# Kernel optimization log

Measured on AMD Instinct MI355X. Metric: run time of the kernel, lower is better.

## Reference

```python
import jax, jax.numpy as jnp
import numpy as np

B, S, D, H = 2, 2048, 1024, 16
HD = D // H
LOCAL_WINDOW = 32
GLOBAL_TOKENS = 16
BLOCK_SIZE = 64
SPARSITY = 0.75


def _structured_mask(seq_len):
    """local_global | block_sparse pattern, vectorized numpy (deterministic)."""
    i = np.arange(seq_len)[:, None]
    j = np.arange(seq_len)[None, :]
    half = LOCAL_WINDOW // 2
    local = np.abs(i - j) <= half  # mask[i, i-16 : i+17]
    glob = (i < GLOBAL_TOKENS) | (j < GLOBAL_TOKENS)
    stride = max(1, seq_len // 64)
    strided = ((i % stride) == 0) & ((j % stride) == 0)
    lg = local | glob | strided
    # block sparse: random blocks kept with prob 1-SPARSITY, diagonal always kept
    nb = (seq_len + BLOCK_SIZE - 1) // BLOCK_SIZE
    rng = np.random.default_rng(0)
    block_mask = rng.random((nb, nb)) > SPARSITY
    np.fill_diagonal(block_mask, True)
    bs = np.kron(block_mask, np.ones((BLOCK_SIZE, BLOCK_SIZE), dtype=bool))[:seq_len, :seq_len]
    return lg | bs


def setup_inputs() -> dict:
    key = jax.random.key(0)
    ks = jax.random.split(key, 12)
    std = 1.0 / np.sqrt(D)
    inp = {
        'query': jax.random.normal(ks[0], (B, S, D), jnp.float32),
        'key': jax.random.normal(ks[1], (B, S, D), jnp.float32),
        'value': jax.random.normal(ks[2], (B, S, D), jnp.float32),
        'Wq': jax.random.normal(ks[3], (D, D), jnp.float32) * std,
        'bq': jnp.zeros((D,), jnp.float32),
        'Wk': jax.random.normal(ks[4], (D, D), jnp.float32) * std,
        'bk': jnp.zeros((D,), jnp.float32),
        'Wv': jax.random.normal(ks[5], (D, D), jnp.float32) * std,
        'bv': jnp.zeros((D,), jnp.float32),
        'Wo': jax.random.normal(ks[6], (D, D), jnp.float32) * std,
        'bo': jnp.zeros((D,), jnp.float32),
        'sparse_mask': jnp.asarray(_structured_mask(S)),
    }
    return inp


def reference(query, key, value, Wq, bq, Wk, bk, Wv, bv, Wo, bo, sparse_mask):
    scale = HD ** -0.5
    # projections -> [B, H, S, HD]
    q = (query @ Wq + bq).reshape(B, S, H, HD).transpose(0, 2, 1, 3)
    k = (key @ Wk + bk).reshape(B, S, H, HD).transpose(0, 2, 1, 3)
    v = (value @ Wv + bv).reshape(B, S, H, HD).transpose(0, 2, 1, 3)
    # dense scores then structured sparse mask (matches original math)
    scores = jnp.einsum('bhqd,bhkd->bhqk', q, k) * scale
    scores = jnp.where(sparse_mask[None, None], scores, -jnp.inf)
    attn = jax.nn.softmax(scores, axis=-1)  # every row has >=1 active entry (global cols)
    out = jnp.einsum('bhqk,bhkd->bhqd', attn, v)
    out = out.transpose(0, 2, 1, 3).reshape(B, S, D)
    out = out @ Wo + bo
    return out, attn
```

## Files before the change

kernel.cpp:

```cpp
#include <hip/hip_runtime.h>
#include <hip/hip_bf16.h>
#include <hip/hip_fp16.h>

using u16 = unsigned short;
using u32 = unsigned int;
using u64 = unsigned long long;

typedef __attribute__((ext_vector_type(8))) short short8;
typedef __attribute__((ext_vector_type(8))) _Float16 half8;
typedef __attribute__((ext_vector_type(4))) _Float16 half4;
typedef __attribute__((ext_vector_type(4))) float f32x4;
typedef __attribute__((ext_vector_type(2))) u32 u32x2;

#define DEVI static __device__ __forceinline__

DEVI float bfu2f(u16 u) { return __builtin_bit_cast(float, (u32)u << 16); }
DEVI u16 f2bfu(float f) { return __builtin_bit_cast(u16, __float2bfloat16(f)); }
DEVI u16 f2hu(float f) { return __builtin_bit_cast(u16, (_Float16)f); }

DEVI f32x4 mfma_f16_(half8 a, half8 b, f32x4 c) {
  return __builtin_amdgcn_mfma_f32_16x16x32_f16(a, b, c, 0, 0, 0);
}
DEVI f32x4 mfma16_f16_(half4 a, half4 b, f32x4 c) {
  return __builtin_amdgcn_mfma_f32_16x16x16f16(a, b, c, 0, 0, 0);
}

#define GLD_LDS16(src, dst) \
  __builtin_amdgcn_global_load_lds((const __attribute__((address_space(1))) void*)(src), \
                                   (__attribute__((address_space(3))) void*)(dst), 16, 0, 0)

#define BAR() __builtin_amdgcn_s_barrier()
#define VMCNT(n) asm volatile("s_waitcnt vmcnt(" #n ")" ::: "memory")

static constexpr int Bsz = 2, S = 2048, D = 1024, H = 16, HD = 64;
static constexpr int MROWS = Bsz * S;
static constexpr size_t OUT_ELEMS = (size_t)Bsz * S * D;
static constexpr float C_EXP2 = 0.18033688f;
static constexpr size_t OFF_WT  = 0;
static constexpr size_t OFF_Q   = 0x800000;
static constexpr size_t OFF_K   = 0x1000000;
static constexpr size_t OFF_V   = 0x1800000;
static constexpr size_t OFF_VT  = 0x2000000;
static constexpr size_t OFF_O   = 0x2800000;
static constexpr size_t OFF_MB  = 0x3000000;
static constexpr size_t OFF_FLG = 0x3080000;

__global__ __launch_bounds__(256) void detect_dtype(
    const u16* __restrict__ q, int* __restrict__ flag)
{
  __shared__ u32 red[256];
  const int tid = threadIdx.x;
  u32 mx = 0;
  for (int i = tid; i < 32768; i += 256) {
    u32 e = (q[2 * i] >> 7) & 0xFF;
    mx = mx > e ? mx : e;
  }
  red[tid] = mx;
  __syncthreads();
  if (tid == 0) {
    u32 m = 0;
    for (int i = 0; i < 256; ++i) m = m > red[i] ? m : red[i];
    flag[0] = (m >= 0x90) ? 1 : 0;
  }
}

__global__ __launch_bounds__(256) void conv_f16(
    const void* __restrict__ X, u16* __restrict__ Y, const int* __restrict__ flag)
{
  const size_t i8 = ((size_t)blockIdx.x * 256 + threadIdx.x) * 8;
  half8 o;
  if (*flag) {
    const float* x = (const float*)X + i8;
    float4 f0 = ((const float4*)x)[0], f1 = ((const float4*)x)[1];
    o[0] = (_Float16)f0.x; o[1] = (_Float16)f0.y;
    o[2] = (_Float16)f0.z; o[3] = (_Float16)f0.w;
    o[4] = (_Float16)f1.x; o[5] = (_Float16)f1.y;
    o[6] = (_Float16)f1.z; o[7] = (_Float16)f1.w;
  } else {
    uint4 a = *(const uint4*)((const u16*)X + i8);
    u32 wd[4] = {a.x, a.y, a.z, a.w};
    #pragma unroll
    for (int j = 0; j < 4; ++j) {
      o[2 * j]     = (_Float16)bfu2f((u16)(wd[j] & 0xFFFF));
      o[2 * j + 1] = (_Float16)bfu2f((u16)(wd[j] >> 16));
    }
  }
  *reinterpret_cast<half8*>(Y + i8) = o;
}

__global__ __launch_bounds__(256) void prep_w(
    const void* __restrict__ Wq, const void* __restrict__ Wk,
    const void* __restrict__ Wv, const void* __restrict__ Wo,
    u16* __restrict__ WT, const int* __restrict__ flag)
{
  __shared__ _Float16 t[64][80];
  const int z = blockIdx.z;
  const void* src = z == 0 ? Wq : z == 1 ? Wk : z == 2 ? Wv : Wo;
  u16* dst = WT + (size_t)z * 1024 * 1024;
  const int bx = blockIdx.x, by = blockIdx.y;
  const int tid = threadIdx.x;
  const int r = tid >> 2, ch = tid & 3;
  const int fl = *flag;
  if (fl) {
    const float* s = (const float*)src + (size_t)(by * 64 + r) * 1024 + bx * 64 + ch * 16;
    #pragma unroll
    for (int v = 0; v < 4; ++v) {
      float4 f = ((const float4*)s)[v];
      t[r][ch * 16 + v * 4 + 0] = (_Float16)f.x;
      t[r][ch * 16 + v * 4 + 1] = (_Float16)f.y;
      t[r][ch * 16 + v * 4 + 2] = (_Float16)f.z;
      t[r][ch * 16 + v * 4 + 3] = (_Float16)f.w;
    }
  } else {
    const u16* s = (const u16*)src + (size_t)(by * 64 + r) * 1024 + bx * 64 + ch * 16;
    uint4 a0 = ((const uint4*)s)[0], a1 = ((const uint4*)s)[1];
    u32 wds[8] = {a0.x, a0.y, a0.z, a0.w, a1.x, a1.y, a1.z, a1.w};
    #pragma unroll
    for (int j = 0; j < 8; ++j) {
      t[r][ch * 16 + 2 * j]     = (_Float16)bfu2f((u16)(wds[j] & 0xFFFF));
      t[r][ch * 16 + 2 * j + 1] = (_Float16)bfu2f((u16)(wds[j] >> 16));
    }
  }
  __syncthreads();
  half8 o0, o1;
  #pragma unroll
  for (int i = 0; i < 8; ++i) { o0[i] = t[ch * 16 + i][r]; o1[i] = t[ch * 16 + 8 + i][r]; }
  u16* d = dst + (size_t)(bx * 64 + r) * 1024 + by * 64 + ch * 16;
  *reinterpret_cast<half8*>(d) = o0;
  *reinterpret_cast<half8*>(d + 8) = o1;
}

__global__ __launch_bounds__(256) void mask_bits_kernel(
    const void* __restrict__ mask, u64* __restrict__ mbits)
{
  const u32 w0 = *(const u32*)mask;
  int mode;
  if (w0 == 0x01010101u) mode = 0;
  else if ((w0 & 0xFFFFu) && (w0 >> 16)) mode = 1;
  else mode = 2;
  const int row = blockIdx.x;
  const int w = threadIdx.x >> 6, l = threadIdx.x & 63;
  for (int i = 0; i < 8; ++i) {
    int jw = w * 8 + i;
    size_t idx = (size_t)row * S + jw * 64 + l;
    bool m;
    if (mode == 0)      m = ((const unsigned char*)mask)[idx] != 0;
    else if (mode == 1) m = ((const u16*)mask)[idx] != 0;
    else                m = ((const u32*)mask)[idx] != 0;
    u64 bal = __ballot(m);
    if (l == 0) mbits[(size_t)row * 32 + jw] = bal;
  }
}

template<int OUT_DYN>
__global__ __launch_bounds__(256) void gemm_f16(
    const _Float16* __restrict__ A, const _Float16* __restrict__ Bt,
    const void* __restrict__ bias, void* __restrict__ C,
    const int* __restrict__ flag, int M, int N, int K)
{
  __shared__ _Float16 As[64 * 64];
  __shared__ _Float16 Bs[128 * 64];
  const int tid = threadIdx.x;
  const int w = tid >> 6, l = tid & 63;
  const int wr = w >> 1, wc = w & 1;
  const int lg = l >> 4, lc = l & 15;
  const int tM = blockIdx.x * 64, tN = blockIdx.y * 128;
  const int fl = *flag;
  const int rr = l >> 3;
  const int gsw = (l & 7) ^ rr;
  const int rsw = lc & 7;

  f32x4 acc[2][4] = {};

  for (int k0 = 0; k0 < K; k0 += 64) {
    #pragma unroll
    for (int s = 0; s < 2; ++s)
      GLD_LDS16(A + (size_t)(tM + w * 16 + s * 8 + rr) * K + k0 + gsw * 8,
                &As[(w * 16 + s * 8) * 64]);
    #pragma unroll
    for (int s = 0; s < 4; ++s)
      GLD_LDS16(Bt + (size_t)(tN + w * 32 + s * 8 + rr) * K + k0 + gsw * 8,
                &Bs[(w * 32 + s * 8) * 64]);
    __syncthreads();
    half8 a[2][2], b[4][2];
    #pragma unroll
    for (int m = 0; m < 2; ++m)
      #pragma unroll
      for (int kk = 0; kk < 2; ++kk)
        a[m][kk] = *reinterpret_cast<const half8*>(
            &As[(wr * 32 + m * 16 + lc) * 64 + ((kk * 4 + lg) ^ rsw) * 8]);
    #pragma unroll
    for (int n = 0; n < 4; ++n)
      #pragma unroll
      for (int kk = 0; kk < 2; ++kk)
        b[n][kk] = *reinterpret_cast<const half8*>(
            &Bs[(wc * 64 + n * 16 + lc) * 64 + ((kk * 4 + lg) ^ rsw) * 8]);
    #pragma unroll
    for (int m = 0; m < 2; ++m)
      #pragma unroll
      for (int n = 0; n < 4; ++n) {
        acc[m][n] = mfma_f16_(a[m][0], b[n][0], acc[m][n]);
        acc[m][n] = mfma_f16_(a[m][1], b[n][1], acc[m][n]);
      }
    __syncthreads();
  }

  float bf[4];
  #pragma unroll
  for (int n = 0; n < 4; ++n) {
    int col = tN + wc * 64 + n * 16 + lc;
    bf[n] = fl ? ((const float*)bias)[col] : bfu2f(((const u16*)bias)[col]);
  }
  #pragma unroll
  for (int m = 0; m < 2; ++m) {
    int row = tM + wr * 32 + m * 16 + lg * 4;
    #pragma unroll
    for (int n = 0; n < 4; ++n) {
      int col = tN + wc * 64 + n * 16 + lc;
      #pragma unroll
      for (int r = 0; r < 4; ++r) {
        float v = acc[m][n][r] + bf[n];
        size_t off = (size_t)(row + r) * N + col;
        if (OUT_DYN) {
          if (fl) ((float*)C)[off] = v;
          else    ((u16*)C)[off] = f2bfu(v);
        } else {
          ((u16*)C)[off] = f2hu(v);
        }
      }
    }
  }
}

__global__ __launch_bounds__(256) void transpose_v(
    const _Float16* __restrict__ V, _Float16* __restrict__ vT)
{
  __shared__ _Float16 t[64][80];
  const int sb = blockIdx.x, bh = blockIdx.y;
  const int b = bh >> 4, h = bh & 15;
  const int tid = threadIdx.x;
  #pragma unroll
  for (int rep = 0; rep < 2; ++rep) {
    int idx = rep * 256 + tid;
    int sl = idx >> 3, ch = idx & 7;
    *reinterpret_cast<uint4*>(&t[sl][ch * 8]) =
      *reinterpret_cast<const uint4*>(V + (size_t)(b * S + sb * 64 + sl) * D + h * HD + ch * 8);
  }
  __syncthreads();
  #pragma unroll
  for (int rep = 0; rep < 2; ++rep) {
    int idx = rep * 256 + tid;
    int hd = idx >> 3, ch = idx & 7;
    half8 ov;
    #pragma unroll
    for (int i = 0; i < 8; ++i) ov[i] = t[ch * 8 + i][hd];
    *reinterpret_cast<half8*>(vT + ((size_t)bh * HD + hd) * S + sb * 64 + ch * 8) = ov;
  }
}

__global__ __launch_bounds__(256) void attn_kernel(
    const _Float16* __restrict__ Q, const _Float16* __restrict__ Kp,
    const _Float16* __restrict__ vT, const u64* __restrict__ mbits,
    _Float16* __restrict__ O, void* __restrict__ dOut,
    const int* __restrict__ flag)
{
  __shared__ _Float16 Ks[2][4096];
  __shared__ _Float16 Vs[2][4096];

  const int tid = threadIdx.x, w = tid >> 6, l = tid & 63;
  const int lg = l >> 4, lc = l & 15;
  const int flat = blockIdx.y * 32 + blockIdx.x;
  const int nf = (flat & 7) * 128 + (flat >> 3);
  const int rb = nf & 31, bh = nf >> 5;
  const int b = bh >> 4, h = bh & 15;
  const int wg = w ^ (rb & 1);
  const int wrow = rb * 64 + wg * 16;
  const int fl = *flag;

  half8 aq[2];
  {
    const _Float16* qp = Q + (size_t)(b * S + wrow + lc) * D + h * HD;
    aq[0] = *reinterpret_cast<const half8*>(qp + lg * 8);
    aq[1] = *reinterpret_cast<const half8*>(qp + 32 + lg * 8);
  }
  const _Float16* kbase = Kp + (size_t)(b * S) * D + h * HD;
  const _Float16* vbase = vT + (size_t)bh * HD * S;
  const u64* mrow = mbits + (size_t)(wrow + lc) * 32;

  const int rr = w * 8 + (l >> 3);
  const int gsw = (l & 7) ^ (rr & 7);

  #define STAGE_K(buf, jb) do { \
    const _Float16* s0_ = kbase + (size_t)((jb) * 64 + rr) * D + gsw * 8; \
    GLD_LDS16(s0_, &Ks[buf][w * 512]); \
    GLD_LDS16(s0_ + (size_t)32 * D, &Ks[buf][2048 + w * 512]); \
  } while (0)
  #define STAGE_V(buf, jb) do { \
    const _Float16* s0_ = vbase + (size_t)rr * S + (jb) * 64 + gsw * 8; \
    GLD_LDS16(s0_, &Vs[buf][w * 512]); \
    GLD_LDS16(s0_ + (size_t)32 * S, &Vs[buf][2048 + w * 512]); \
  } while (0)

  const int sw = lc & 7;

  float rs = 0.f;
  f32x4 accO[4] = {};

  STAGE_K(0, 0);
  STAGE_V(0, 0);
  u64 mb = mrow[0];

  #pragma unroll 1
  for (int jb = 0; jb < 32; ++jb) {
    const int buf = jb & 1;
    BAR();
    if (jb < 31) {
      STAGE_K(buf ^ 1, jb + 1);
      STAGE_V(buf ^ 1, jb + 1);
      VMCNT(5);
    } else {
      VMCNT(1);
    }
    BAR();
    const u64 mb_next = (jb < 31) ? mrow[jb + 1] : 0ull;
    const _Float16* kt = Ks[buf];
    const _Float16* vt = Vs[buf];
    #pragma unroll
    for (int c = 0; c < 4; ++c) {
      const u32 bits = (u32)(mb >> (c * 16 + lg * 4)) & 0xFu;
      if (__any(bits != 0)) {
        const int r = c * 16 + lc;
        half8 ka = *reinterpret_cast<const half8*>(&kt[r * 64 + ((lg ^ sw) * 8)]);
        half8 kb = *reinterpret_cast<const half8*>(&kt[r * 64 + (((lg + 4) ^ sw) * 8)]);
        f32x4 sc = {};
        sc = mfma_f16_(ka, aq[0], sc);
        sc = mfma_f16_(kb, aq[1], sc);
        half4 pa;
        #pragma unroll
        for (int r2 = 0; r2 < 4; ++r2) {
          float p = ((bits >> r2) & 1) ? exp2f(sc[r2] * C_EXP2) : 0.f;
          rs += p;
          pa[r2] = (_Float16)p;
        }
        #pragma unroll
        for (int d = 0; d < 4; ++d) {
          const int rd = d * 16 + lc;
          const int ch = (2 * c + (lg >> 1)) ^ sw;
          half4 vv = *reinterpret_cast<const half4*>(&vt[rd * 64 + ch * 8 + (lg & 1) * 4]);
          accO[d] = mfma16_f16_(pa, vv, accO[d]);
        }
      }
    }
    mb = mb_next;
  }

  rs += __shfl_xor(rs, 16);
  rs += __shfl_xor(rs, 32);
  const float inv = 1.f / rs;
  const float lg2i = -__log2f(rs);

  float invr[4];
  #pragma unroll
  for (int r = 0; r < 4; ++r) invr[r] = __shfl(inv, lg * 4 + r);

  {
    _Float16* op = O + (size_t)(b * S + wrow + lg * 4) * D + h * HD;
    #pragma unroll
    for (int d = 0; d < 4; ++d)
      #pragma unroll
      for (int r = 0; r < 4; ++r)
        op[(size_t)r * D + d * 16 + lc] = (_Float16)(accO[d][r] * invr[r]);
  }

  STAGE_K(0, 0);
  mb = mrow[0];

  if (fl) {
    float* ar = (float*)dOut + OUT_ELEMS + (size_t)bh * S * S + (size_t)(wrow + lc) * S;
    #pragma unroll 1
    for (int jb = 0; jb < 32; ++jb) {
      const int buf = jb & 1;
      BAR();
      if (jb < 31) { STAGE_K(buf ^ 1, jb + 1); VMCNT(7); }
      else VMCNT(5);
      BAR();
      const u64 mb_next = (jb < 31) ? mrow[jb + 1] : 0ull;
      const _Float16* kt = Ks[buf];
      #pragma unroll
      for (int c = 0; c < 4; ++c) {
        const u32 bits = (u32)(mb >> (c * 16 + lg * 4)) & 0xFu;
        f32x4* dst = (f32x4*)(ar + jb * 64 + c * 16 + lg * 4);
        if (__any(bits != 0)) {
          const int r = c * 16 + lc;
          half8 ka = *reinterpret_cast<const half8*>(&kt[r * 64 + ((lg ^ sw) * 8)]);
          half8 kb = *reinterpret_cast<const half8*>(&kt[r * 64 + (((lg + 4) ^ sw) * 8)]);
          f32x4 sc = {};
          sc = mfma_f16_(ka, aq[0], sc);
          sc = mfma_f16_(kb, aq[1], sc);
          f32x4 pv;
          #pragma unroll
          for (int r2 = 0; r2 < 4; ++r2)
            pv[r2] = ((bits >> r2) & 1) ? exp2f(__builtin_fmaf(sc[r2], C_EXP2, lg2i)) : 0.f;
          __builtin_nontemporal_store(pv, dst);
        } else {
          f32x4 z = {};
          __builtin_nontemporal_store(z, dst);
        }
      }
      mb = mb_next;
    }
  } else {
    u16* ar = (u16*)dOut + OUT_ELEMS + (size_t)bh * S * S + (size_t)(wrow + lc) * S;
    #pragma unroll 1
    for (int jb = 0; jb < 32; ++jb) {
      const int buf = jb & 1;
      BAR();
      if (jb < 31) { STAGE_K(buf ^ 1, jb + 1); VMCNT(7); }
      else VMCNT(5);
      BAR();
      const u64 mb_next = (jb < 31) ? mrow[jb + 1] : 0ull;
      const _Float16* kt = Ks[buf];
      #pragma unroll
      for (int c = 0; c < 4; ++c) {
        const u32 bits = (u32)(mb >> (c * 16 + lg * 4)) & 0xFu;
        u32x2* dst = (u32x2*)(ar + jb * 64 + c * 16 + lg * 4);
        if (__any(bits != 0)) {
          const int r = c * 16 + lc;
          half8 ka = *reinterpret_cast<const half8*>(&kt[r * 64 + ((lg ^ sw) * 8)]);
          half8 kb = *reinterpret_cast<const half8*>(&kt[r * 64 + (((lg + 4) ^ sw) * 8)]);
          f32x4 sc = {};
          sc = mfma_f16_(ka, aq[0], sc);
          sc = mfma_f16_(kb, aq[1], sc);
          float p0 = ((bits >> 0) & 1) ? exp2f(__builtin_fmaf(sc[0], C_EXP2, lg2i)) : 0.f;
          float p1 = ((bits >> 1) & 1) ? exp2f(__builtin_fmaf(sc[1], C_EXP2, lg2i)) : 0.f;
          float p2 = ((bits >> 2) & 1) ? exp2f(__builtin_fmaf(sc[2], C_EXP2, lg2i)) : 0.f;
          float p3 = ((bits >> 3) & 1) ? exp2f(__builtin_fmaf(sc[3], C_EXP2, lg2i)) : 0.f;
          u32x2 pk;
          pk[0] = (u32)f2bfu(p0) | ((u32)f2bfu(p1) << 16);
          pk[1] = (u32)f2bfu(p2) | ((u32)f2bfu(p3) << 16);
          __builtin_nontemporal_store(pk, dst);
        } else {
          u32x2 z = {0, 0};
          __builtin_nontemporal_store(z, dst);
        }
      }
      mb = mb_next;
    }
  }
  #undef STAGE_K
  #undef STAGE_V
}

extern "C" void kernel_launch(void* const* d_in, const int* in_sizes, int n_in,
                              void* d_out, int out_size, void* d_ws, size_t ws_size,
                              hipStream_t stream) {
  const void* query = d_in[0];
  const void* key_  = d_in[1];
  const void* value = d_in[2];
  const void* Wq = d_in[3];  const void* bq = d_in[4];
  const void* Wk = d_in[5];  const void* bk = d_in[6];
  const void* Wv = d_in[7];  const void* bv = d_in[8];
  const void* Wo = d_in[9];  const void* bo = d_in[10];
  const void* mask = d_in[11];

  char* ws = (char*)d_ws;
  u16* WT   = (u16*)(ws + OFF_WT);
  u16* Qb   = (u16*)(ws + OFF_Q);
  u16* Kb   = (u16*)(ws + OFF_K);
  u16* Vb   = (u16*)(ws + OFF_V);
  u16* vTb  = (u16*)(ws + OFF_VT);
  u16* Ob   = (u16*)(ws + OFF_O);
  u64* mbits = (u64*)(ws + OFF_MB);
  int* flag  = (int*)(ws + OFF_FLG);

  u16* WqT = WT, *WkT = WT + 1048576, *WvT = WT + 2097152, *WoT = WT + 3145728;
  u16* X = vTb;

  detect_dtype<<<1, 256, 0, stream>>>((const u16*)query, flag);
  prep_w<<<dim3(16, 16, 4), 256, 0, stream>>>(Wq, Wk, Wv, Wo, WT, flag);
  mask_bits_kernel<<<dim3(S), 256, 0, stream>>>(mask, mbits);

  const dim3 gg(MROWS / 64, D / 128);
  conv_f16<<<dim3(2048), 256, 0, stream>>>(query, X, flag);
  gemm_f16<0><<<gg, 256, 0, stream>>>((const _Float16*)X, (const _Float16*)WqT,
                                      bq, Qb, flag, MROWS, D, D);
  conv_f16<<<dim3(2048), 256, 0, stream>>>(key_, X, flag);
  gemm_f16<0><<<gg, 256, 0, stream>>>((const _Float16*)X, (const _Float16*)WkT,
                                      bk, Kb, flag, MROWS, D, D);
  conv_f16<<<dim3(2048), 256, 0, stream>>>(value, X, flag);
  gemm_f16<0><<<gg, 256, 0, stream>>>((const _Float16*)X, (const _Float16*)WvT,
                                      bv, Vb, flag, MROWS, D, D);

  transpose_v<<<dim3(32, 32), 256, 0, stream>>>((const _Float16*)Vb, (_Float16*)vTb);
  attn_kernel<<<dim3(32, 32), 256, 0, stream>>>(
      (const _Float16*)Qb, (const _Float16*)Kb, (const _Float16*)vTb,
      mbits, (_Float16*)Ob, d_out, flag);
  gemm_f16<1><<<gg, 256, 0, stream>>>((const _Float16*)Ob, (const _Float16*)WoT,
                                      bo, d_out, flag, MROWS, D, D);
}
```

Before: 344.9 us.

## Fuse input dtype conversion into a single batched QKV projection GEMM

The three separate conversion kernels and three projection GEMMs become one launch with a z-dimension of three. Each block converts fp32/bf16 activations to fp16 in registers and writes them straight into swizzled LDS, so the converted copy no longer makes a round trip through global memory. The A-tile load now goes through plain register loads instead of direct-to-LDS loads, which may lose some latency hiding. Separately, the attention-probability output stores switch from nontemporal to regular stores.

```diff
diff --git a/kernel.cpp b/kernel.cpp
--- a/kernel.cpp
+++ b/kernel.cpp
@@ -62,30 +62,6 @@
     for (int i = 0; i < 256; ++i) m = m > red[i] ? m : red[i];
     flag[0] = (m >= 0x90) ? 1 : 0;
   }
-}
-
-__global__ __launch_bounds__(256) void conv_f16(
-    const void* __restrict__ X, u16* __restrict__ Y, const int* __restrict__ flag)
-{
-  const size_t i8 = ((size_t)blockIdx.x * 256 + threadIdx.x) * 8;
-  half8 o;
-  if (*flag) {
-    const float* x = (const float*)X + i8;
-    float4 f0 = ((const float4*)x)[0], f1 = ((const float4*)x)[1];
-    o[0] = (_Float16)f0.x; o[1] = (_Float16)f0.y;
-    o[2] = (_Float16)f0.z; o[3] = (_Float16)f0.w;
-    o[4] = (_Float16)f1.x; o[5] = (_Float16)f1.y;
-    o[6] = (_Float16)f1.z; o[7] = (_Float16)f1.w;
-  } else {
-    uint4 a = *(const uint4*)((const u16*)X + i8);
-    u32 wd[4] = {a.x, a.y, a.z, a.w};
-    #pragma unroll
-    for (int j = 0; j < 4; ++j) {
-      o[2 * j]     = (_Float16)bfu2f((u16)(wd[j] & 0xFFFF));
-      o[2 * j + 1] = (_Float16)bfu2f((u16)(wd[j] >> 16));
-    }
-  }
-  *reinterpret_cast<half8*>(Y + i8) = o;
 }
 
 __global__ __launch_bounds__(256) void prep_w(
@@ -152,31 +128,59 @@
   }
 }
 
-template<int OUT_DYN>
-__global__ __launch_bounds__(256) void gemm_f16(
-    const _Float16* __restrict__ A, const _Float16* __restrict__ Bt,
-    const void* __restrict__ bias, void* __restrict__ C,
-    const int* __restrict__ flag, int M, int N, int K)
-{
-  __shared__ _Float16 As[64 * 64];
-  __shared__ _Float16 Bs[128 * 64];
+template<int A_DYN, int OUT_DYN>
+DEVI void gemm_body(const void* __restrict__ A, const _Float16* __restrict__ Bt,
+                    const void* __restrict__ bias, void* __restrict__ C,
+                    int fl, int tM, int tN, int N, int K,
+                    _Float16* As, _Float16* Bs)
+{
   const int tid = threadIdx.x;
   const int w = tid >> 6, l = tid & 63;
   const int wr = w >> 1, wc = w & 1;
   const int lg = l >> 4, lc = l & 15;
-  const int tM = blockIdx.x * 64, tN = blockIdx.y * 128;
-  const int fl = *flag;
   const int rr = l >> 3;
   const int gsw = (l & 7) ^ rr;
   const int rsw = lc & 7;
+  const int arow = tid >> 2, ach = tid & 3;
 
   f32x4 acc[2][4] = {};
 
   for (int k0 = 0; k0 < K; k0 += 64) {
-    #pragma unroll
-    for (int s = 0; s < 2; ++s)
-      GLD_LDS16(A + (size_t)(tM + w * 16 + s * 8 + rr) * K + k0 + gsw * 8,
-                &As[(w * 16 + s * 8) * 64]);
+    if (A_DYN) {
+      half8 h0, h1;
+      if (fl) {
+        const float* ap = (const float*)A + (size_t)(tM + arow) * K + k0 + ach * 16;
+        float4 f0 = ((const float4*)ap)[0], f1 = ((const float4*)ap)[1];
+        float4 f2 = ((const float4*)ap)[2], f3 = ((const float4*)ap)[3];
+        h0[0] = (_Float16)f0.x; h0[1] = (_Float16)f0.y;
+        h0[2] = (_Float16)f0.z; h0[3] = (_Float16)f0.w;
+        h0[4] = (_Float16)f1.x; h0[5] = (_Float16)f1.y;
+        h0[6] = (_Float16)f1.z; h0[7] = (_Float16)f1.w;
+        h1[0] = (_Float16)f2.x; h1[1] = (_Float16)f2.y;
+        h1[2] = (_Float16)f2.z; h1[3] = (_Float16)f2.w;
+        h1[4] = (_Float16)f3.x; h1[5] = (_Float16)f3.y;
+        h1[6] = (_Float16)f3.z; h1[7] = (_Float16)f3.w;
+      } else {
+        const u16* ap = (const u16*)A + (size_t)(tM + arow) * K + k0 + ach * 16;
+        uint4 a0 = ((const uint4*)ap)[0], a1 = ((const uint4*)ap)[1];
+        u32 wd[8] = {a0.x, a0.y, a0.z, a0.w, a1.x, a1.y, a1.z, a1.w};
+        #pragma unroll
+        for (int j = 0; j < 4; ++j) {
+          h0[2 * j]     = (_Float16)bfu2f((u16)(wd[j] & 0xFFFF));
+          h0[2 * j + 1] = (_Float16)bfu2f((u16)(wd[j] >> 16));
+          h1[2 * j]     = (_Float16)bfu2f((u16)(wd[4 + j] & 0xFFFF));
+          h1[2 * j + 1] = (_Float16)bfu2f((u16)(wd[4 + j] >> 16));
+        }
+      }
+      const int c0 = (2 * ach) ^ (arow & 7), c1 = (2 * ach + 1) ^ (arow & 7);
+      *reinterpret_cast<half8*>(&As[arow * 64 + c0 * 8]) = h0;
+      *reinterpret_cast<half8*>(&As[arow * 64 + c1 * 8]) = h1;
+    } else {
+      #pragma unroll
+      for (int s = 0; s < 2; ++s)
+        GLD_LDS16((const _Float16*)A + (size_t)(tM + w * 16 + s * 8 + rr) * K + k0 + gsw * 8,
+                  &As[(w * 16 + s * 8) * 64]);
+    }
     #pragma unroll
     for (int s = 0; s < 4; ++s)
       GLD_LDS16(Bt + (size_t)(tN + w * 32 + s * 8 + rr) * K + k0 + gsw * 8,
@@ -230,6 +234,36 @@
       }
     }
   }
+}
+
+__global__ __launch_bounds__(256) void gemm_qkv(
+    const void* __restrict__ Aq, const void* __restrict__ Ak,
+    const void* __restrict__ Av, const u16* __restrict__ WT,
+    const void* __restrict__ bq, const void* __restrict__ bk,
+    const void* __restrict__ bv,
+    u16* __restrict__ Qb, u16* __restrict__ Kb, u16* __restrict__ Vb,
+    const int* __restrict__ flag)
+{
+  __shared__ _Float16 As[64 * 64];
+  __shared__ _Float16 Bs[128 * 64];
+  const int z = blockIdx.z;
+  const void* A = z == 0 ? Aq : z == 1 ? Ak : Av;
+  const _Float16* Bt = (const _Float16*)(WT + (size_t)z * 1048576);
+  const void* bias = z == 0 ? bq : z == 1 ? bk : bv;
+  void* C = z == 0 ? Qb : z == 1 ? Kb : Vb;
+  gemm_body<1, 0>(A, Bt, bias, C, *flag,
+                  blockIdx.x * 64, blockIdx.y * 128, D, D, As, Bs);
+}
+
+__global__ __launch_bounds__(256) void gemm_o(
+    const _Float16* __restrict__ A, const u16* __restrict__ WoT,
+    const void* __restrict__ bias, void* __restrict__ C,
+    const int* __restrict__ flag)
+{
+  __shared__ _Float16 As[64 * 64];
+  __shared__ _Float16 Bs[128 * 64];
+  gemm_body<0, 1>(A, (const _Float16*)WoT, bias, C, *flag,
+                  blockIdx.x * 64, blockIdx.y * 128, D, D, As, Bs);
 }
 
 __global__ __launch_bounds__(256) void transpose_v(
@@ -401,10 +435,10 @@
           #pragma unroll
           for (int r2 = 0; r2 < 4; ++r2)
             pv[r2] = ((bits >> r2) & 1) ? exp2f(__builtin_fmaf(sc[r2], C_EXP2, lg2i)) : 0.f;
-          __builtin_nontemporal_store(pv, dst);
+          *dst = pv;
         } else {
           f32x4 z = {};
-          __builtin_nontemporal_store(z, dst);
+          *dst = z;
         }
       }
       mb = mb_next;
@@ -438,10 +472,10 @@
           u32x2 pk;
           pk[0] = (u32)f2bfu(p0) | ((u32)f2bfu(p1) << 16);
           pk[1] = (u32)f2bfu(p2) | ((u32)f2bfu(p3) << 16);
-          __builtin_nontemporal_store(pk, dst);
+          *dst = pk;
         } else {
           u32x2 z = {0, 0};
-          __builtin_nontemporal_store(z, dst);
+          *dst = z;
         }
       }
       mb = mb_next;
@@ -473,28 +507,19 @@
   u64* mbits = (u64*)(ws + OFF_MB);
   int* flag  = (int*)(ws + OFF_FLG);
 
-  u16* WqT = WT, *WkT = WT + 1048576, *WvT = WT + 2097152, *WoT = WT + 3145728;
-  u16* X = vTb;
+  u16* WoT = WT + 3145728;
 
   detect_dtype<<<1, 256, 0, stream>>>((const u16*)query, flag);
   prep_w<<<dim3(16, 16, 4), 256, 0, stream>>>(Wq, Wk, Wv, Wo, WT, flag);
   mask_bits_kernel<<<dim3(S), 256, 0, stream>>>(mask, mbits);
 
-  const dim3 gg(MROWS / 64, D / 128);
-  conv_f16<<<dim3(2048), 256, 0, stream>>>(query, X, flag);
-  gemm_f16<0><<<gg, 256, 0, stream>>>((const _Float16*)X, (const _Float16*)WqT,
-                                      bq, Qb, flag, MROWS, D, D);
-  conv_f16<<<dim3(2048), 256, 0, stream>>>(key_, X, flag);
-  gemm_f16<0><<<gg, 256, 0, stream>>>((const _Float16*)X, (const _Float16*)WkT,
-                                      bk, Kb, flag, MROWS, D, D);
-  conv_f16<<<dim3(2048), 256, 0, stream>>>(value, X, flag);
-  gemm_f16<0><<<gg, 256, 0, stream>>>((const _Float16*)X, (const _Float16*)WvT,
-                                      bv, Vb, flag, MROWS, D, D);
+  gemm_qkv<<<dim3(MROWS / 64, D / 128, 3), 256, 0, stream>>>(
+      query, key_, value, WT, bq, bk, bv, Qb, Kb, Vb, flag);
 
   transpose_v<<<dim3(32, 32), 256, 0, stream>>>((const _Float16*)Vb, (_Float16*)vTb);
   attn_kernel<<<dim3(32, 32), 256, 0, stream>>>(
       (const _Float16*)Qb, (const _Float16*)Kb, (const _Float16*)vTb,
       mbits, (_Float16*)Ob, d_out, flag);
-  gemm_f16<1><<<gg, 256, 0, stream>>>((const _Float16*)Ob, (const _Float16*)WoT,
-                                      bo, d_out, flag, MROWS, D, D);
-}
+  gemm_o<<<dim3(MROWS / 64, D / 128), 256, 0, stream>>>(
+      (const _Float16*)Ob, WoT, bo, d_out, flag);
+}
```

Result: faster. 326.3 us, median of 2 (-5.4%).
